# Performance work log

Hardware: AMD Instinct MI355X
Metric: run time of the kernel (lower is better)

The kernel has to match this reference:

```python
import jax, jax.numpy as jnp
import numpy as np

B, L, D = 4, 2048, 2048
S, K, NB = 16, 4, 2
H = D // 64  # num_heads = 32
EPS = 1e-6


def _rms(x, w):
    return x * jax.lax.rsqrt(jnp.mean(x * x, axis=-1, keepdims=True) + EPS) * w


def setup_inputs() -> dict:
    key = jax.random.key(0)
    ks = jax.random.split(key, 8)
    g = lambda k, shape, s: jax.random.normal(k, shape, dtype=jnp.float32) * s
    return {
        'x': g(ks[0], (B, L, D), 1.0),
        'workspace': g(ks[1], (S, D), 0.02),
        'compete_w': g(ks[2], (S, D), 0.02),
        'compete_b': jnp.zeros((S,), jnp.float32),
        'write_w': g(ks[3], (D, D), 0.02),
        'write_b': jnp.zeros((D,), jnp.float32),
        'in_proj_w': g(ks[4], (3 * D, D), 0.02),
        'in_proj_b': jnp.zeros((3 * D,), jnp.float32),
        'out_proj_w': g(ks[5], (D, D), 0.02),
        'out_proj_b': jnp.zeros((D,), jnp.float32),
        'ig_w': g(ks[6], (1, D), 0.02),
        'ig_b': jnp.zeros((1,), jnp.float32),
        'norm_pre_w': jnp.ones((D,), jnp.float32),
        'norm_post_w': jnp.ones((D,), jnp.float32),
    }


def reference(x, workspace, compete_w, compete_b, write_w, write_b,
              in_proj_w, in_proj_b, out_proj_w, out_proj_b,
              ig_w, ig_b, norm_pre_w, norm_post_w):
    Bq, Lq, Dd = x.shape
    hd = Dd // H
    scale = 1.0 / np.sqrt(hd).astype(np.float32)
    ws = jnp.broadcast_to(workspace[None], (Bq, S, Dd))
    wq, wk, wv = in_proj_w[:Dd], in_proj_w[Dd:2 * Dd], in_proj_w[2 * Dd:]
    bq, bk, bv = in_proj_b[:Dd], in_proj_b[Dd:2 * Dd], in_proj_b[2 * Dd:]
    k_eff = min(K, Lq)
    for _ in range(NB):  # n_broadcasts is small & structural
        # slot competition: top-k tokens per slot over the L axis
        logits = _rms(x, norm_pre_w) @ compete_w.T + compete_b       # [B,L,S]
        slot_logits = jnp.swapaxes(logits, 1, 2)                     # [B,S,L]
        vals, idx = jax.lax.top_k(slot_logits, k_eff)                # [B,S,k]
        wgt = jax.nn.softmax(vals, axis=-1)                          # [B,S,k]
        # scatter-softmax + bmm == gather winning tokens and weight-sum
        wx = x @ write_w.T + write_b                                 # [B,L,D]
        gathered = jnp.take_along_axis(wx[:, None], idx[..., None], axis=2)  # [B,S,k,D]
        written = jnp.einsum('bsk,bskd->bsd', wgt, gathered)         # [B,S,D]
        ws = _rms(ws + written, norm_post_w)
        # cross-attention broadcast: tokens query the 16 workspace slots
        q = (x @ wq.T + bq).reshape(Bq, Lq, H, hd)
        kk = (ws @ wk.T + bk).reshape(Bq, S, H, hd)
        vv = (ws @ wv.T + bv).reshape(Bq, S, H, hd)
        att = jax.nn.softmax(jnp.einsum('blhd,bshd->bhls', q, kk) * scale, axis=-1)
        ctx = jnp.einsum('bhls,bshd->blhd', att, vv).reshape(Bq, Lq, Dd)
        x_b = ctx @ out_proj_w.T + out_proj_b
        x = _rms(x + x_b, norm_post_w)
        # ignition head (aux scalar output per token)
        ignition = jax.nn.sigmoid(x @ ig_w.T + ig_b)  # [B,L,1]
    return x
```

## Files before the change

### kernel.cpp

```cpp
#include <hip/hip_runtime.h>
#include <stdint.h>

#define D 2048
#define LSEQ 2048
#define BATCH 4
#define BL (BATCH * LSEQ)
#define NSLOT 16
#define NHEAD 32
#define HDIM 64
#define EPSV 1e-6f

typedef __attribute__((ext_vector_type(8))) short bf16x8;
typedef __attribute__((ext_vector_type(4))) float f32x4;

static __device__ __forceinline__ ushort f2bf(float f) {
    uint32_t u = __float_as_uint(f);
    u += 0x7fffu + ((u >> 16) & 1u);
    return (ushort)(u >> 16);
}

template <int CTRL>
static __device__ __forceinline__ float dpp_xadd(float v) {
    int t = __builtin_amdgcn_mov_dpp(__float_as_int(v), CTRL, 0xf, 0xf, true);
    return v + __int_as_float(t);
}

static __device__ __forceinline__ float wave_sum(float v) {
    v += __shfl_xor(v, 32, 64);
    v += __shfl_xor(v, 16, 64);
    v = dpp_xadd<0x128>(v);
    v += __shfl_xor(v, 4, 64);
    v = dpp_xadd<0x4E>(v);
    v = dpp_xadd<0xB1>(v);
    return v;
}

static __device__ __forceinline__ void gl_lds16(const void* g, void* l) {
    __builtin_amdgcn_global_load_lds(
        (__attribute__((address_space(1))) uint32_t*)(uintptr_t)g,
        (__attribute__((address_space(3))) uint32_t*)(uint32_t)(uintptr_t)l,
        16, 0, 0);
}

__global__ __launch_bounds__(256) void conv_bf16_kernel(const float4* __restrict__ src,
                                                        ushort* __restrict__ dst, int n4) {
    int i = blockIdx.x * 256 + threadIdx.x;
    int stride = gridDim.x * 256;
    for (; i < n4; i += stride) {
        float4 v = src[i];
        uint2 o;
        o.x = (uint)f2bf(v.x) | ((uint)f2bf(v.y) << 16);
        o.y = (uint)f2bf(v.z) | ((uint)f2bf(v.w) << 16);
        *(uint2*)(dst + (size_t)i * 4) = o;
    }
}

__global__ __launch_bounds__(256) void transpose_bf16_kernel(const ushort* __restrict__ src,
                                                             ushort* __restrict__ dst) {
    __shared__ ushort t[64][72];
    int bx = blockIdx.x & 31, by = blockIdx.x >> 5;
    int r0 = by * 64, c0 = bx * 64;
    int tid = threadIdx.x;
    int lr = tid >> 3;
    int lc = (tid & 7) * 8;
#pragma unroll
    for (int p = 0; p < 2; ++p) {
        int rr = p * 32 + lr;
        bf16x8 v = *(const bf16x8*)(src + (size_t)(r0 + rr) * 2048 + c0 + lc);
#pragma unroll
        for (int j = 0; j < 8; ++j) t[lc + j][rr] = (ushort)v[j];
    }
    __syncthreads();
#pragma unroll
    for (int p = 0; p < 2; ++p) {
        int rr = p * 32 + lr;
        *(bf16x8*)(dst + (size_t)(c0 + rr) * 2048 + r0 + lc) = *(const bf16x8*)&t[rr][lc];
    }
}

__global__ __launch_bounds__(256) void logits_kernel(
    const float* __restrict__ x, const float* __restrict__ cw,
    const float* __restrict__ cb, const float* __restrict__ wpre,
    float* __restrict__ logits_t) {
    int blk = blockIdx.x;
    int b = blk >> 9;
    int l0 = (blk & 511) << 2;
    int tid = threadIdx.x;
    int i0 = tid * 8;
    float4 w0 = *(const float4*)(wpre + i0);
    float4 w1 = *(const float4*)(wpre + i0 + 4);
    float wv[8] = {w0.x, w0.y, w0.z, w0.w, w1.x, w1.y, w1.z, w1.w};
    float xw[4][8];
    float ss[4];
#pragma unroll
    for (int r = 0; r < 4; ++r) {
        const float* xr = x + ((size_t)(b * LSEQ + l0 + r)) * D;
        float4 a0 = *(const float4*)(xr + i0);
        float4 a1 = *(const float4*)(xr + i0 + 4);
        float xv[8] = {a0.x, a0.y, a0.z, a0.w, a1.x, a1.y, a1.z, a1.w};
        float s0 = 0.f;
#pragma unroll
        for (int j = 0; j < 8; ++j) { s0 += xv[j] * xv[j]; xw[r][j] = xv[j] * wv[j]; }
        ss[r] = s0;
    }
#pragma unroll
    for (int r = 0; r < 4; ++r) ss[r] = wave_sum(ss[r]);
    __shared__ float red[4][NSLOT][4];
    __shared__ float redss[4][4];
    int lane = tid & 63, w = tid >> 6;
    if (lane == 0) {
#pragma unroll
        for (int r = 0; r < 4; ++r) redss[w][r] = ss[r];
    }
#pragma unroll 2
    for (int s = 0; s < NSLOT; ++s) {
        const float* cwr = cw + (size_t)s * D + i0;
        float4 c0 = *(const float4*)(cwr);
        float4 c1 = *(const float4*)(cwr + 4);
        float acc[4];
#pragma unroll
        for (int r = 0; r < 4; ++r)
            acc[r] = xw[r][0] * c0.x + xw[r][1] * c0.y + xw[r][2] * c0.z + xw[r][3] * c0.w +
                     xw[r][4] * c1.x + xw[r][5] * c1.y + xw[r][6] * c1.z + xw[r][7] * c1.w;
#pragma unroll
        for (int r = 0; r < 4; ++r) acc[r] = wave_sum(acc[r]);
        if (lane == 0) {
#pragma unroll
            for (int r = 0; r < 4; ++r) red[w][s][r] = acc[r];
        }
    }
    __syncthreads();
    if (tid < 64) {
        int s = tid >> 2, r = tid & 3;
        float tot = red[0][s][r] + red[1][s][r] + red[2][s][r] + red[3][s][r];
        float s2 = redss[0][r] + redss[1][r] + redss[2][r] + redss[3][r];
        float rsq = 1.0f / sqrtf(s2 * (1.0f / (float)D) + EPSV);
        logits_t[((size_t)(b * NSLOT + s)) * LSEQ + l0 + r] = tot * rsq + cb[s];
    }
}

__global__ __launch_bounds__(256) void topk_xbar_kernel(
    const float* __restrict__ logits_t, const float* __restrict__ x,
    ushort* __restrict__ xbar_b) {
    int bs = blockIdx.x;
    int b = bs >> 4;
    const float* lr = logits_t + (size_t)bs * LSEQ;
    int tid = threadIdx.x, lane = tid & 63, w = tid >> 6;
    __shared__ float rv[4];
    __shared__ int ri[4];
    __shared__ float selv[4];
    __shared__ int seli[4];
    int i0 = tid * 8;
    float myv[8];
#pragma unroll
    for (int j = 0; j < 8; ++j) myv[j] = lr[i0 + j];
    int chosen[4];
    for (int p = 0; p < 4; ++p) {
        float bv = -3.4e38f;
        int bi = 0x7fffffff;
#pragma unroll
        for (int j = 0; j < 8; ++j) {
            int i = i0 + j;
            bool skip = false;
            for (int q = 0; q < p; ++q) skip = skip || (i == chosen[q]);
            float v = myv[j];
            if (!skip && (v > bv || (v == bv && i < bi))) { bv = v; bi = i; }
        }
#pragma unroll
        for (int off = 1; off < 64; off <<= 1) {
            float ov = __shfl_xor(bv, off, 64);
            int oi = __shfl_xor(bi, off, 64);
            if (ov > bv || (ov == bv && oi < bi)) { bv = ov; bi = oi; }
        }
        if (lane == 0) { rv[w] = bv; ri[w] = bi; }
        __syncthreads();
        if (tid == 0) {
            float fv = rv[0];
            int fi = ri[0];
            for (int q = 1; q < 4; ++q)
                if (rv[q] > fv || (rv[q] == fv && ri[q] < fi)) { fv = rv[q]; fi = ri[q]; }
            selv[p] = fv;
            seli[p] = fi;
        }
        __syncthreads();
        chosen[p] = seli[p];
    }
    float vals[4];
#pragma unroll
    for (int p = 0; p < 4; ++p) vals[p] = selv[p];
    float mx = vals[0];
    float e[4], den = 0.f;
#pragma unroll
    for (int p = 0; p < 4; ++p) { e[p] = expf(vals[p] - mx); den += e[p]; }
    float inv = 1.0f / den;
    const float* xr0 = x + ((size_t)b * LSEQ + chosen[0]) * D;
    const float* xr1 = x + ((size_t)b * LSEQ + chosen[1]) * D;
    const float* xr2 = x + ((size_t)b * LSEQ + chosen[2]) * D;
    const float* xr3 = x + ((size_t)b * LSEQ + chosen[3]) * D;
    float s[8];
#pragma unroll
    for (int j = 0; j < 8; ++j) {
        int i = i0 + j;
        s[j] = (e[0] * xr0[i] + e[1] * xr1[i] + e[2] * xr2[i] + e[3] * xr3[i]) * inv;
    }
    uint4 o;
    o.x = (uint)f2bf(s[0]) | ((uint)f2bf(s[1]) << 16);
    o.y = (uint)f2bf(s[2]) | ((uint)f2bf(s[3]) << 16);
    o.z = (uint)f2bf(s[4]) | ((uint)f2bf(s[5]) << 16);
    o.w = (uint)f2bf(s[6]) | ((uint)f2bf(s[7]) << 16);
    *(uint4*)(xbar_b + (size_t)bs * D + i0) = o;
}

__global__ __launch_bounds__(256) void ws_update_kernel(
    const float* __restrict__ written, const float* __restrict__ ws_prev,
    const float* __restrict__ workspace0, int first,
    const float* __restrict__ wpost, float* __restrict__ ws_out,
    ushort* __restrict__ ws_b) {
    int bs = blockIdx.x;
    int s = bs & (NSLOT - 1);
    int tid = threadIdx.x;
    int i0 = tid * 8;
    const float* prev = first ? (workspace0 + (size_t)s * D) : (ws_prev + (size_t)bs * D);
    const float* wr = written + (size_t)bs * D;
    float4 p0 = *(const float4*)(prev + i0);
    float4 p1 = *(const float4*)(prev + i0 + 4);
    float4 q0 = *(const float4*)(wr + i0);
    float4 q1 = *(const float4*)(wr + i0 + 4);
    float t[8] = {p0.x + q0.x, p0.y + q0.y, p0.z + q0.z, p0.w + q0.w,
                  p1.x + q1.x, p1.y + q1.y, p1.z + q1.z, p1.w + q1.w};
    float ss = 0.f;
#pragma unroll
    for (int j = 0; j < 8; ++j) ss += t[j] * t[j];
    ss = wave_sum(ss);
    __shared__ float sb[4];
    if ((tid & 63) == 0) sb[tid >> 6] = ss;
    __syncthreads();
    ss = sb[0] + sb[1] + sb[2] + sb[3];
    float rsq = 1.0f / sqrtf(ss * (1.0f / (float)D) + EPSV);
    float4 w0 = *(const float4*)(wpost + i0);
    float4 w1 = *(const float4*)(wpost + i0 + 4);
    float wv[8] = {w0.x, w0.y, w0.z, w0.w, w1.x, w1.y, w1.z, w1.w};
    float o[8];
#pragma unroll
    for (int j = 0; j < 8; ++j) o[j] = t[j] * rsq * wv[j];
    float4 r0 = {o[0], o[1], o[2], o[3]};
    float4 r1 = {o[4], o[5], o[6], o[7]};
    *(float4*)(ws_out + (size_t)bs * D + i0) = r0;
    *(float4*)(ws_out + (size_t)bs * D + i0 + 4) = r1;
    uint4 ob;
    ob.x = (uint)f2bf(o[0]) | ((uint)f2bf(o[1]) << 16);
    ob.y = (uint)f2bf(o[2]) | ((uint)f2bf(o[3]) << 16);
    ob.z = (uint)f2bf(o[4]) | ((uint)f2bf(o[5]) << 16);
    ob.w = (uint)f2bf(o[6]) | ((uint)f2bf(o[7]) << 16);
    *(uint4*)(ws_b + (size_t)bs * D + i0) = ob;
}

__global__ __launch_bounds__(256) void resid_rms_kernel(
    const float* __restrict__ x_src, const ushort* __restrict__ ao,
    const float* __restrict__ wpost, float* __restrict__ x_dst,
    ushort* __restrict__ xb) {
    int row = blockIdx.x;
    int tid = threadIdx.x;
    int i0 = tid * 8;
    const float* xr = x_src + (size_t)row * D;
    uint4 av = *(const uint4*)(ao + (size_t)row * D + i0);
    float af[8];
    af[0] = __uint_as_float(av.x << 16);
    af[1] = __uint_as_float(av.x & 0xffff0000u);
    af[2] = __uint_as_float(av.y << 16);
    af[3] = __uint_as_float(av.y & 0xffff0000u);
    af[4] = __uint_as_float(av.z << 16);
    af[5] = __uint_as_float(av.z & 0xffff0000u);
    af[6] = __uint_as_float(av.w << 16);
    af[7] = __uint_as_float(av.w & 0xffff0000u);
    float4 p0 = *(const float4*)(xr + i0);
    float4 p1 = *(const float4*)(xr + i0 + 4);
    float t[8] = {p0.x + af[0], p0.y + af[1], p0.z + af[2], p0.w + af[3],
                  p1.x + af[4], p1.y + af[5], p1.z + af[6], p1.w + af[7]};
    float ss = 0.f;
#pragma unroll
    for (int j = 0; j < 8; ++j) ss += t[j] * t[j];
    ss = wave_sum(ss);
    __shared__ float sb[4];
    if ((tid & 63) == 0) sb[tid >> 6] = ss;
    __syncthreads();
    ss = sb[0] + sb[1] + sb[2] + sb[3];
    float rsq = 1.0f / sqrtf(ss * (1.0f / (float)D) + EPSV);
    float4 w0 = *(const float4*)(wpost + i0);
    float4 w1 = *(const float4*)(wpost + i0 + 4);
    float wv[8] = {w0.x, w0.y, w0.z, w0.w, w1.x, w1.y, w1.z, w1.w};
    float o[8];
#pragma unroll
    for (int j = 0; j < 8; ++j) o[j] = t[j] * rsq * wv[j];
    float4 r0 = {o[0], o[1], o[2], o[3]};
    float4 r1 = {o[4], o[5], o[6], o[7]};
    *(float4*)(x_dst + (size_t)row * D + i0) = r0;
    *(float4*)(x_dst + (size_t)row * D + i0 + 4) = r1;
    uint4 ob;
    ob.x = (uint)f2bf(o[0]) | ((uint)f2bf(o[1]) << 16);
    ob.y = (uint)f2bf(o[2]) | ((uint)f2bf(o[3]) << 16);
    ob.z = (uint)f2bf(o[4]) | ((uint)f2bf(o[5]) << 16);
    ob.w = (uint)f2bf(o[6]) | ((uint)f2bf(o[7]) << 16);
    *(uint4*)(xb + (size_t)row * D + i0) = ob;
}

template <int TRANS>
static __device__ __forceinline__ void grouped16_body(
    int blk, const ushort* __restrict__ Abase, const ushort* __restrict__ Bmat,
    ushort* __restrict__ Cout) {
    int g = blk >> 3;
    int nt = blk & 7;
    int h = g & 31;
    int hoff = h * 64;
    int tid = threadIdx.x, lane = tid & 63, wv = tid >> 6;
    int j0 = nt * 256 + wv * 64;
    int rr = lane & 15, ko = lane >> 4;
    const ushort* A = Abase + (size_t)g * 16 * 64;
    bf16x8 af0 = *(const bf16x8*)(A + rr * 64 + ko * 8);
    bf16x8 af1 = *(const bf16x8*)(A + rr * 64 + 32 + ko * 8);
    f32x4 acc[4];
    f32x4 zero = {0.f, 0.f, 0.f, 0.f};
#pragma unroll
    for (int nf = 0; nf < 4; ++nf) acc[nf] = zero;
#pragma unroll
    for (int nf = 0; nf < 4; ++nf) {
        int j = j0 + nf * 16 + rr;
        bf16x8 b0 = *(const bf16x8*)(Bmat + (size_t)j * 2048 + hoff + ko * 8);
        bf16x8 b1 = *(const bf16x8*)(Bmat + (size_t)j * 2048 + hoff + 32 + ko * 8);
        acc[nf] = __builtin_amdgcn_mfma_f32_16x16x32_bf16(af0, b0, acc[nf], 0, 0, 0);
        acc[nf] = __builtin_amdgcn_mfma_f32_16x16x32_bf16(af1, b1, acc[nf], 0, 0, 0);
    }
#pragma unroll
    for (int nf = 0; nf < 4; ++nf)
#pragma unroll
        for (int r = 0; r < 4; ++r) {
            int s = ko * 4 + r;
            int j = j0 + nf * 16 + rr;
            ushort v = f2bf(acc[nf][r]);
            if (TRANS) Cout[(size_t)j * 2048 + g * 16 + s] = v;
            else       Cout[(size_t)(g * 16 + s) * 2048 + j] = v;
        }
}

__global__ __launch_bounds__(256) void fused_prep_kernel(
    const ushort* __restrict__ kb16, const ushort* __restrict__ vb16,
    const float* __restrict__ bq, const ushort* __restrict__ wqt,
    const ushort* __restrict__ wob, ushort* __restrict__ ktil,
    ushort* __restrict__ wtilT, float* __restrict__ cbias) {
    int blk = blockIdx.x;
    if (blk < 1024) {
        grouped16_body<0>(blk, kb16, wqt, ktil);
    } else if (blk < 2048) {
        grouped16_body<1>(blk - 1024, vb16, wob, wtilT);
    } else {
        int i = (blk - 2048) * 256 + threadIdx.x;
        int hs = i & 511;
        int h = hs >> 4;
        const ushort* kr = kb16 + (size_t)i * 64;
        const float* bb = bq + h * 64;
        float acc = 0.f;
#pragma unroll
        for (int d = 0; d < 64; ++d)
            acc += __uint_as_float(((uint)kr[d]) << 16) * bb[d];
        cbias[i] = acc;
    }
}

__global__ __launch_bounds__(256) void attn_sm_kernel(
    const float* __restrict__ qlog, const float* __restrict__ cb,
    ushort* __restrict__ aatt) {
    int blk = blockIdx.x;
    int tid = threadIdx.x;
    int l = blk * 8 + (tid >> 5);
    int b = l >> 11;
    int h = tid & 31;
    const float* q0 = qlog + (size_t)l * 512 + h * 16;
    const float* q1 = q0 + (size_t)BL * 512;
    const float* c = cb + b * 512 + h * 16;
    float p[16];
#pragma unroll
    for (int i = 0; i < 16; i += 4) {
        float4 v0 = *(const float4*)(q0 + i);
        float4 v1 = *(const float4*)(q1 + i);
        float4 cc = *(const float4*)(c + i);
        p[i]     = v0.x + v1.x + cc.x;
        p[i + 1] = v0.y + v1.y + cc.y;
        p[i + 2] = v0.z + v1.z + cc.z;
        p[i + 3] = v0.w + v1.w + cc.w;
    }
    float mx = p[0];
#pragma unroll
    for (int s = 1; s < 16; ++s) mx = fmaxf(mx, p[s]);
    float den = 0.f;
#pragma unroll
    for (int s = 0; s < 16; ++s) { p[s] = __expf((p[s] - mx) * 0.125f); den += p[s]; }
    float inv = 1.0f / den;
    uint4 o[2];
    uint* ow = (uint*)o;
#pragma unroll
    for (int i = 0; i < 8; ++i)
        ow[i] = (uint)f2bf(p[2 * i] * inv) | ((uint)f2bf(p[2 * i + 1] * inv) << 16);
    ushort* dst = aatt + (size_t)l * 512 + h * 16;
    *(uint4*)dst = o[0];
    *(uint4*)(dst + 8) = o[1];
}

template <int KVMODE>
__global__ __launch_bounds__(256) void gemm_tiny(
    const ushort* __restrict__ A, const ushort* __restrict__ Bw,
    const float* __restrict__ bias, float* __restrict__ C,
    int M, int N, int K, ushort* __restrict__ kvk, ushort* __restrict__ kvv) {
    int gw = (blockIdx.x * 256 + threadIdx.x) >> 6;
    int lane = threadIdx.x & 63;
    int ntiles = N >> 4;
    int nt = gw % ntiles, mt = gw / ntiles;
    int rr = lane & 15, ko = lane >> 4;
    const ushort* Ar = A + (size_t)(mt * 16 + rr) * K;
    const ushort* Br = Bw + (size_t)(nt * 16 + rr) * K;
    f32x4 acc = {0.f, 0.f, 0.f, 0.f};
    int NT = K / 32;
#pragma unroll 8
    for (int t = 0; t < NT; ++t) {
        bf16x8 af = *(const bf16x8*)(Ar + t * 32 + ko * 8);
        bf16x8 bf = *(const bf16x8*)(Br + t * 32 + ko * 8);
        acc = __builtin_amdgcn_mfma_f32_16x16x32_bf16(af, bf, acc, 0, 0, 0);
    }
    int col = nt * 16 + rr;
    float bsv = bias ? bias[col] : 0.f;
#pragma unroll
    for (int r = 0; r < 4; ++r) {
        int rowi = mt * 16 + ko * 4 + r;
        float v = acc[r] + bsv;
        if (KVMODE) {
            int b = rowi >> 4, s = rowi & 15;
            int c2 = (col < 2048) ? col : col - 2048;
            int h = c2 >> 6, d = c2 & 63;
            size_t dst = (((size_t)(b * NHEAD + h)) * NSLOT + s) * HDIM + d;
            if (col < 2048) kvk[dst] = f2bf(v);
            else            kvv[dst] = f2bf(v);
        } else {
            C[(size_t)rowi * N + col] = v;
        }
    }
}

template <int BM, int OBF>
__global__ __launch_bounds__(256) void gemm_bt(
    const ushort* __restrict__ A, const ushort* __restrict__ Bw,
    const float* __restrict__ bias, float* __restrict__ C,
    int M, int N, int K, size_t bOff, int bStride, int aStride,
    int zA, int zB, size_t zC) {
    constexpr int BN = 128, BK = 32;
    constexpr int MF = BM / 32;
    constexpr int APASS = (BM * BK / 8) / 256;
    __shared__ short lds[2][(BM + BN) * BK];
    int tid = threadIdx.x;
    int lane = tid & 63, w = tid >> 6;
    int wr = w >> 1, wc = w & 1;
    int tn = blockIdx.x * BN;
    int tm = blockIdx.y * BM;
    int ksl = blockIdx.z;
    A += (size_t)ksl * zA;
    Bw += (size_t)ksl * zB + (size_t)(tm >> 11) * bOff;
    C += (size_t)ksl * zC;
    f32x4 acc[MF][4];
    f32x4 zero = {0.f, 0.f, 0.f, 0.f};
#pragma unroll
    for (int m = 0; m < MF; ++m)
#pragma unroll
        for (int n = 0; n < 4; ++n) acc[m][n] = zero;
    int NT = K / BK;

    auto stage = [&](int buf, int t) {
        int kt = t * BK;
#pragma unroll
        for (int p = 0; p < APASS; ++p) {
            int cb = p * 256 + w * 64;
            int c = cb + lane;
            int r = c >> 2;
            int k8 = (c & 3) * 8;
            int gr = tm + r;
            if (gr >= M) gr = M - 1;
            gl_lds16(A + (size_t)gr * aStride + kt + k8, (void*)&lds[buf][cb * 8]);
        }
#pragma unroll
        for (int p = 0; p < 2; ++p) {
            int cb = p * 256 + w * 64;
            int c = cb + lane;
            int r = c >> 2;
            int k8 = (c & 3) * 8;
            gl_lds16(Bw + (size_t)(tn + r) * bStride + kt + k8,
                     (void*)&lds[buf][BM * BK + cb * 8]);
        }
    };
    stage(0, 0);
    for (int t = 0; t < NT; ++t) {
        __syncthreads();
        if (t + 1 < NT) stage((t + 1) & 1, t + 1);
        const short* Ab = &lds[t & 1][0];
        const short* Bb = &lds[t & 1][BM * BK];
        int ko = (lane >> 4) * 8;
        int rr = lane & 15;
        bf16x8 af[MF], bfr[4];
#pragma unroll
        for (int m = 0; m < MF; ++m)
            af[m] = *(const bf16x8*)&Ab[(wr * (MF * 16) + m * 16 + rr) * BK + ko];
#pragma unroll
        for (int n = 0; n < 4; ++n)
            bfr[n] = *(const bf16x8*)&Bb[(wc * 64 + n * 16 + rr) * BK + ko];
#pragma unroll
        for (int m = 0; m < MF; ++m)
#pragma unroll
            for (int n = 0; n < 4; ++n)
                acc[m][n] = __builtin_amdgcn_mfma_f32_16x16x32_bf16(af[m], bfr[n],
                                                                    acc[m][n], 0, 0, 0);
    }
#pragma unroll
    for (int m = 0; m < MF; ++m) {
#pragma unroll
        for (int n = 0; n < 4; ++n) {
            int col = tn + wc * 64 + n * 16 + (lane & 15);
            float bsv = bias ? bias[col] : 0.f;
#pragma unroll
            for (int r = 0; r < 4; ++r) {
                int rowi = tm + wr * (MF * 16) + m * 16 + (lane >> 4) * 4 + r;
                if (rowi >= M) continue;
                float v = acc[m][n][r] + bsv;
                if (OBF) ((ushort*)C)[(size_t)rowi * N + col] = f2bf(v);
                else     C[(size_t)rowi * N + col] = v;
            }
        }
    }
}

extern "C" void kernel_launch(void* const* d_in, const int* in_sizes, int n_in,
                              void* d_out, int out_size, void* d_ws, size_t ws_size,
                              hipStream_t stream) {
    const float* x_in       = (const float*)d_in[0];
    const float* workspace  = (const float*)d_in[1];
    const float* compete_w  = (const float*)d_in[2];
    const float* compete_b  = (const float*)d_in[3];
    const float* write_w    = (const float*)d_in[4];
    const float* write_b    = (const float*)d_in[5];
    const float* in_proj_w  = (const float*)d_in[6];
    const float* in_proj_b  = (const float*)d_in[7];
    const float* out_proj_w = (const float*)d_in[8];
    const float* out_proj_b = (const float*)d_in[9];
    const float* norm_pre_w  = (const float*)d_in[12];
    const float* norm_post_w = (const float*)d_in[13];
    float* xout = (float*)d_out;

    char* base = (char*)d_ws;
    size_t off = 0;
    auto alloc = [&](size_t bytes) {
        void* p = base + off;
        off += (bytes + 255) & ~(size_t)255;
        return p;
    };
    ushort* xb      = (ushort*)alloc((size_t)BL * D * 2);
    ushort* xbb     = (ushort*)alloc((size_t)BL * D * 2);
    float*  logits  = (float*) alloc((size_t)BATCH * NSLOT * LSEQ * 4);
    ushort* xbar    = (ushort*)alloc((size_t)BATCH * NSLOT * D * 2);
    float*  written = (float*) alloc((size_t)BATCH * NSLOT * D * 4);
    float*  wsbuf   = (float*) alloc((size_t)BATCH * NSLOT * D * 4);
    ushort* wsb     = (ushort*)alloc((size_t)BATCH * NSLOT * D * 2);
    ushort* ipb     = (ushort*)alloc((size_t)3 * D * D * 2);
    ushort* wob     = (ushort*)alloc((size_t)D * D * 2);
    ushort* wwb     = (ushort*)alloc((size_t)D * D * 2);
    ushort* wqt     = (ushort*)alloc((size_t)D * D * 2);
    ushort* kb16    = (ushort*)alloc((size_t)BATCH * NHEAD * NSLOT * HDIM * 2);
    ushort* vb16    = (ushort*)alloc((size_t)BATCH * NHEAD * NSLOT * HDIM * 2);
    ushort* ktil    = (ushort*)alloc((size_t)BATCH * 512 * D * 2);
    ushort* wtilT   = (ushort*)alloc((size_t)D * BATCH * 512 * 2);
    float*  qlog    = (float*) alloc((size_t)2 * BL * 512 * 4);
    ushort* aatt    = (ushort*)alloc((size_t)BL * 512 * 2);
    float*  cbias   = (float*) alloc((size_t)BATCH * 512 * 4);
    (void)ws_size; (void)in_sizes; (void)n_in; (void)out_size;

    conv_bf16_kernel<<<2048, 256, 0, stream>>>((const float4*)in_proj_w, ipb, 3 * D * D / 4);
    conv_bf16_kernel<<<2048, 256, 0, stream>>>((const float4*)out_proj_w, wob, D * D / 4);
    conv_bf16_kernel<<<2048, 256, 0, stream>>>((const float4*)write_w, wwb, D * D / 4);
    conv_bf16_kernel<<<2048, 256, 0, stream>>>((const float4*)x_in, xb, BL * D / 4);
    transpose_bf16_kernel<<<1024, 256, 0, stream>>>(ipb, wqt);

    for (int it = 0; it < 2; ++it) {
        const float* xs = it ? (const float*)xout : x_in;
        logits_kernel<<<BL / 4, 256, 0, stream>>>(xs, compete_w, compete_b, norm_pre_w,
                                                  logits);
        topk_xbar_kernel<<<BATCH * NSLOT, 256, 0, stream>>>(logits, xs, xbar);
        gemm_tiny<0><<<128, 256, 0, stream>>>(xbar, wwb, write_b, written,
                                              BATCH * NSLOT, D, D,
                                              (ushort*)nullptr, (ushort*)nullptr);
        ws_update_kernel<<<BATCH * NSLOT, 256, 0, stream>>>(written, wsbuf, workspace,
                                                            it == 0 ? 1 : 0, norm_post_w,
                                                            wsbuf, wsb);
        gemm_tiny<1><<<256, 256, 0, stream>>>(wsb, ipb + (size_t)D * D, in_proj_b + D,
                                              (float*)nullptr, BATCH * NSLOT, 2 * D, D,
                                              kb16, vb16);
        fused_prep_kernel<<<2056, 256, 0, stream>>>(kb16, vb16, in_proj_b, wqt, wob,
                                                    ktil, wtilT, cbias);
        gemm_bt<64, 0><<<dim3(512 / 128, BL / 64, 2), 256, 0, stream>>>(
            xb, ktil, (const float*)nullptr, qlog, BL, 512, D / 2,
            (size_t)512 * D, D, D, D / 2, D / 2, (size_t)BL * 512);
        attn_sm_kernel<<<BL / 8, 256, 0, stream>>>(qlog, cbias, aatt);
        gemm_bt<64, 1><<<dim3(D / 128, BL / 64), 256, 0, stream>>>(
            aatt, wtilT, out_proj_b, (float*)xbb, BL, D, 512,
            (size_t)512, D, 512, 0, 0, 0);
        resid_rms_kernel<<<BL, 256, 0, stream>>>(xs, xbb, norm_post_w, xout, xb);
    }
}
```

Measured before the change: 496.4 us.

## Store split-K query logits as bf16 and swizzle GEMM LDS layout

New measurement: 486.4 us. 2.0% less time.

```diff
diff --git a/kernel.cpp b/kernel.cpp
--- a/kernel.cpp
+++ b/kernel.cpp
@@ -367,26 +367,31 @@
 }
 
 __global__ __launch_bounds__(256) void attn_sm_kernel(
-    const float* __restrict__ qlog, const float* __restrict__ cb,
+    const ushort* __restrict__ qlog, const float* __restrict__ cb,
     ushort* __restrict__ aatt) {
     int blk = blockIdx.x;
     int tid = threadIdx.x;
     int l = blk * 8 + (tid >> 5);
     int b = l >> 11;
     int h = tid & 31;
-    const float* q0 = qlog + (size_t)l * 512 + h * 16;
-    const float* q1 = q0 + (size_t)BL * 512;
+    const ushort* q0 = qlog + (size_t)l * 512 + h * 16;
+    const ushort* q1 = q0 + (size_t)BL * 512;
     const float* c = cb + b * 512 + h * 16;
+    uint4 u0a = *(const uint4*)q0;
+    uint4 u0b = *(const uint4*)(q0 + 8);
+    uint4 u1a = *(const uint4*)q1;
+    uint4 u1b = *(const uint4*)(q1 + 8);
+    uint ua[8] = {u0a.x, u0a.y, u0a.z, u0a.w, u0b.x, u0b.y, u0b.z, u0b.w};
+    uint ub[8] = {u1a.x, u1a.y, u1a.z, u1a.w, u1b.x, u1b.y, u1b.z, u1b.w};
     float p[16];
 #pragma unroll
-    for (int i = 0; i < 16; i += 4) {
-        float4 v0 = *(const float4*)(q0 + i);
-        float4 v1 = *(const float4*)(q1 + i);
-        float4 cc = *(const float4*)(c + i);
-        p[i]     = v0.x + v1.x + cc.x;
-        p[i + 1] = v0.y + v1.y + cc.y;
-        p[i + 2] = v0.z + v1.z + cc.z;
-        p[i + 3] = v0.w + v1.w + cc.w;
+    for (int i = 0; i < 8; ++i) {
+        float a0 = __uint_as_float(ua[i] << 16);
+        float a1 = __uint_as_float(ua[i] & 0xffff0000u);
+        float b0 = __uint_as_float(ub[i] << 16);
+        float b1 = __uint_as_float(ub[i] & 0xffff0000u);
+        p[2 * i]     = a0 + b0 + c[2 * i];
+        p[2 * i + 1] = a1 + b1 + c[2 * i + 1];
     }
     float mx = p[0];
 #pragma unroll
@@ -477,8 +482,10 @@
         for (int p = 0; p < APASS; ++p) {
             int cb = p * 256 + w * 64;
             int c = cb + lane;
-            int r = c >> 2;
-            int k8 = (c & 3) * 8;
+            int L = c >> 3, slot = c & 7;
+            int lc = slot ^ (L & 7);
+            int r = 2 * L + (lc >> 2);
+            int k8 = (lc & 3) * 8;
             int gr = tm + r;
             if (gr >= M) gr = M - 1;
             gl_lds16(A + (size_t)gr * aStride + kt + k8, (void*)&lds[buf][cb * 8]);
@@ -487,8 +494,10 @@
         for (int p = 0; p < 2; ++p) {
             int cb = p * 256 + w * 64;
             int c = cb + lane;
-            int r = c >> 2;
-            int k8 = (c & 3) * 8;
+            int L = c >> 3, slot = c & 7;
+            int lc = slot ^ (L & 7);
+            int r = 2 * L + (lc >> 2);
+            int k8 = (lc & 3) * 8;
             gl_lds16(Bw + (size_t)(tn + r) * bStride + kt + k8,
                      (void*)&lds[buf][BM * BK + cb * 8]);
         }
@@ -499,15 +508,23 @@
         if (t + 1 < NT) stage((t + 1) & 1, t + 1);
         const short* Ab = &lds[t & 1][0];
         const short* Bb = &lds[t & 1][BM * BK];
-        int ko = (lane >> 4) * 8;
+        int kc = lane >> 4;
         int rr = lane & 15;
         bf16x8 af[MF], bfr[4];
 #pragma unroll
-        for (int m = 0; m < MF; ++m)
-            af[m] = *(const bf16x8*)&Ab[(wr * (MF * 16) + m * 16 + rr) * BK + ko];
-#pragma unroll
-        for (int n = 0; n < 4; ++n)
-            bfr[n] = *(const bf16x8*)&Bb[(wc * 64 + n * 16 + rr) * BK + ko];
+        for (int m = 0; m < MF; ++m) {
+            int row = wr * (MF * 16) + m * 16 + rr;
+            int L = row >> 1;
+            int sl = (((row & 1) * 4 + kc)) ^ (L & 7);
+            af[m] = *(const bf16x8*)&Ab[L * 64 + sl * 8];
+        }
+#pragma unroll
+        for (int n = 0; n < 4; ++n) {
+            int row = wc * 64 + n * 16 + rr;
+            int L = row >> 1;
+            int sl = (((row & 1) * 4 + kc)) ^ (L & 7);
+            bfr[n] = *(const bf16x8*)&Bb[L * 64 + sl * 8];
+        }
 #pragma unroll
         for (int m = 0; m < MF; ++m)
 #pragma unroll
@@ -572,7 +589,7 @@
     ushort* vb16    = (ushort*)alloc((size_t)BATCH * NHEAD * NSLOT * HDIM * 2);
     ushort* ktil    = (ushort*)alloc((size_t)BATCH * 512 * D * 2);
     ushort* wtilT   = (ushort*)alloc((size_t)D * BATCH * 512 * 2);
-    float*  qlog    = (float*) alloc((size_t)2 * BL * 512 * 4);
+    ushort* qlogb   = (ushort*)alloc((size_t)2 * BL * 512 * 2);
     ushort* aatt    = (ushort*)alloc((size_t)BL * 512 * 2);
     float*  cbias   = (float*) alloc((size_t)BATCH * 512 * 4);
     (void)ws_size; (void)in_sizes; (void)n_in; (void)out_size;
@@ -599,10 +616,10 @@
                                               kb16, vb16);
         fused_prep_kernel<<<2056, 256, 0, stream>>>(kb16, vb16, in_proj_b, wqt, wob,
                                                     ktil, wtilT, cbias);
-        gemm_bt<64, 0><<<dim3(512 / 128, BL / 64, 2), 256, 0, stream>>>(
-            xb, ktil, (const float*)nullptr, qlog, BL, 512, D / 2,
-            (size_t)512 * D, D, D, D / 2, D / 2, (size_t)BL * 512);
-        attn_sm_kernel<<<BL / 8, 256, 0, stream>>>(qlog, cbias, aatt);
+        gemm_bt<64, 1><<<dim3(512 / 128, BL / 64, 2), 256, 0, stream>>>(
+            xb, ktil, (const float*)nullptr, (float*)qlogb, BL, 512, D / 2,
+            (size_t)512 * D, D, D, D / 2, D / 2, (size_t)(BL * 512 / 2));
+        attn_sm_kernel<<<BL / 8, 256, 0, stream>>>(qlogb, cbias, aatt);
         gemm_bt<64, 1><<<dim3(D / 128, BL / 64), 256, 0, stream>>>(
             aatt, wtilT, out_proj_b, (float*)xbb, BL, D, 512,
             (size_t)512, D, 512, 0, 0, 0);
```
